# Optimization experiments

Measured on AMD Instinct MI355X. Metric: run time of the kernel, lower is better.

The kernel has to match this reference:

```python
import jax, jax.numpy as jnp
import numpy as np

EMBED = 768
FFN = 3072
HEADS = 12
HEAD_DIM = EMBED // HEADS
B, T = 4, 2048


def _layer_norm(x, g, b, eps=1e-5):
    m = jnp.mean(x, axis=-1, keepdims=True)
    v = jnp.mean((x - m) ** 2, axis=-1, keepdims=True)
    return (x - m) * jax.lax.rsqrt(v + eps) * g + b


def setup_inputs() -> dict:
    key = jax.random.key(0)
    ks = jax.random.split(key, 8)
    s_e = 1.0 / np.sqrt(EMBED)
    s_f = 1.0 / np.sqrt(FFN)
    # weights stored [in, out] (transpose of torch Linear layout)
    return {
        "x": jax.random.normal(ks[0], (B, T, EMBED), dtype=jnp.float32),
        "ln1_g": jnp.ones((EMBED,), jnp.float32),
        "ln1_b": jnp.zeros((EMBED,), jnp.float32),
        "wq": jax.random.uniform(ks[1], (EMBED, EMBED), jnp.float32, -s_e, s_e),
        "bq": jnp.zeros((EMBED,), jnp.float32),
        "wk": jax.random.uniform(ks[2], (EMBED, EMBED), jnp.float32, -s_e, s_e),
        "bk": jnp.zeros((EMBED,), jnp.float32),
        "wv": jax.random.uniform(ks[3], (EMBED, EMBED), jnp.float32, -s_e, s_e),
        "bv": jnp.zeros((EMBED,), jnp.float32),
        "wo": jax.random.uniform(ks[4], (EMBED, EMBED), jnp.float32, -s_e, s_e),
        "bo": jnp.zeros((EMBED,), jnp.float32),
        "ln2_g": jnp.ones((EMBED,), jnp.float32),
        "ln2_b": jnp.zeros((EMBED,), jnp.float32),
        "w1": jax.random.uniform(ks[5], (EMBED, FFN), jnp.float32, -s_e, s_e),
        "b1": jnp.zeros((FFN,), jnp.float32),
        "w2": jax.random.uniform(ks[6], (FFN, EMBED), jnp.float32, -s_f, s_f),
        "b2": jnp.zeros((EMBED,), jnp.float32),
    }


def reference(x, ln1_g, ln1_b, wq, bq, wk, bk, wv, bv, wo, bo,
              ln2_g, ln2_b, w1, b1, w2, b2):
    Bx, Tx, C = x.shape
    # --- self-attention block (pre-norm) ---
    residual = x
    h = _layer_norm(x, ln1_g, ln1_b)
    q = (h @ wq + bq).reshape(Bx, Tx, HEADS, HEAD_DIM)
    k = (h @ wk + bk).reshape(Bx, Tx, HEADS, HEAD_DIM)
    v = (h @ wv + bv).reshape(Bx, Tx, HEADS, HEAD_DIM)
    scale = 1.0 / np.sqrt(HEAD_DIM)
    attn = jnp.einsum('bqhd,bkhd->bhqk', q, k) * scale  # [B,H,T,T]
    attn = jax.nn.softmax(attn, axis=-1)
    o = jnp.einsum('bhqk,bkhd->bqhd', attn, v).reshape(Bx, Tx, C)
    x = residual + (o @ wo + bo)
    # --- FFN block (pre-norm) ---
    residual = x
    h = _layer_norm(x, ln2_g, ln2_b)
    h = jax.nn.gelu(h @ w1 + b1, approximate=False)
    x = residual + (h @ w2 + b2)
    return x
```

## Files before the change

kernel.cpp:

```cpp
#include <hip/hip_runtime.h>
#include <hip/hip_bf16.h>

#define EMBED 768
#define FFNDIM 3072
#define HEADS 12
#define HDIM  64
#define BB    4
#define TT    2048
#define MTOK  (BB*TT)

typedef __hip_bfloat16 bf16;
typedef __attribute__((ext_vector_type(8))) short short8;
typedef __attribute__((ext_vector_type(4))) float f32x4;
typedef __attribute__((ext_vector_type(16))) float f32x16;
typedef __attribute__((ext_vector_type(4))) unsigned short ushort4v;

__device__ __forceinline__ f32x4 mfma16(short8 a, short8 b, f32x4 c) {
  return __builtin_amdgcn_mfma_f32_16x16x32_bf16(a, b, c, 0, 0, 0);
}
__device__ __forceinline__ f32x16 mfma32(short8 a, short8 b, f32x16 c) {
  return __builtin_amdgcn_mfma_f32_32x32x16_bf16(a, b, c, 0, 0, 0);
}

__device__ __forceinline__ unsigned short f2bf(float f) {
  union { float f; unsigned int u; } v; v.f = f;
  unsigned int u = v.u;
  return (unsigned short)((u + 0x7fffu + ((u >> 16) & 1u)) >> 16);
}

__device__ __forceinline__ float fexp2(float x) {
#if __has_builtin(__builtin_amdgcn_exp2f)
  return __builtin_amdgcn_exp2f(x);
#else
  return exp2f(x);
#endif
}

__device__ __forceinline__ float gelu_f(float v) {
  const float ax = fabsf(v) * 0.70710678118f;
  const float t = __builtin_amdgcn_rcpf(1.f + 0.3275911f * ax);
  float p = 1.061405429f;
  p = p * t - 1.453152027f;
  p = p * t + 1.421413741f;
  p = p * t - 0.284496736f;
  p = p * t + 0.254829592f;
  p = p * t;
  const float e = fexp2(-ax * ax * 1.4426950408889634f);
  float er = 1.f - p * e;
  er = (v < 0.f) ? -er : er;
  return 0.5f * v * (1.f + er);
}

__device__ __forceinline__ unsigned cvtpk(float lo, float hi) {
  unsigned r;
  asm("v_cvt_pk_bf16_f32 %0, %1, %2" : "=v"(r) : "v"(lo), "v"(hi));
  return r;
}
__device__ __forceinline__ void pl32swap(unsigned& vdst, unsigned& vsrc) {
  asm("v_permlane32_swap_b32 %0, %1" : "+v"(vdst), "+v"(vsrc));
}

__device__ __forceinline__ void gl_lds16(const void* g, void* l) {
  __builtin_amdgcn_global_load_lds((const __attribute__((address_space(1))) void*)g,
                                   (__attribute__((address_space(3))) void*)l, 16, 0, 0);
}

template <int N>
__device__ __forceinline__ void wait_vm() {
  asm volatile("s_waitcnt vmcnt(%0)" :: "i"(N) : "memory");
  __builtin_amdgcn_sched_barrier(0);
}
__device__ __forceinline__ void block_barrier() {
  __builtin_amdgcn_sched_barrier(0);
  __builtin_amdgcn_s_barrier();
  __builtin_amdgcn_sched_barrier(0);
}

#define QSCALE 0.18033688011112042f
#define DEFER_THR 11.54f

struct TArgs {
  const float* src[6];
  bf16* dst[6];
  int K[6];
  int N[6];
};

__global__ __launch_bounds__(256) void transpose_k(TArgs ta) {
  const int mi = blockIdx.z;
  const int K = ta.K[mi], N = ta.N[mi];
  const int nt = N / 32;
  const int bx = blockIdx.x % nt, by = blockIdx.x / nt;
  const int n0 = bx * 32, k0 = by * 32;
  if (k0 >= K) return;
  __shared__ float t[32][33];
  const float* __restrict__ W = ta.src[mi];
  bf16* __restrict__ Wt = ta.dst[mi];
  const int tx = threadIdx.x & 31, ty = threadIdx.x >> 5;
#pragma unroll
  for (int i = 0; i < 4; ++i) {
    int kk = ty + i * 8;
    t[tx][kk] = W[(size_t)(k0 + kk) * N + n0 + tx];
  }
  __syncthreads();
#pragma unroll
  for (int i = 0; i < 4; ++i) {
    int nn = ty + i * 8;
    Wt[(size_t)(n0 + nn) * K + k0 + tx] = __float2bfloat16(t[nn][tx]);
  }
}

__global__ __launch_bounds__(256) void ln_k(const float* __restrict__ x,
                                            const float* __restrict__ g,
                                            const float* __restrict__ b,
                                            bf16* __restrict__ out) {
  const int row = blockIdx.x * 4 + (threadIdx.x >> 6);
  const int lane = threadIdx.x & 63;
  const float* xr = x + (size_t)row * EMBED;
  float4 v[3];
  float s = 0.f;
#pragma unroll
  for (int i = 0; i < 3; ++i) {
    v[i] = *(const float4*)&xr[i * 256 + lane * 4];
    s += v[i].x + v[i].y + v[i].z + v[i].w;
  }
#pragma unroll
  for (int m = 1; m < 64; m <<= 1) s += __shfl_xor(s, m);
  const float mean = s * (1.f / 768.f);
  float ss = 0.f;
#pragma unroll
  for (int i = 0; i < 3; ++i) {
    float dx = v[i].x - mean, dy = v[i].y - mean, dz = v[i].z - mean, dw = v[i].w - mean;
    ss += dx * dx + dy * dy + dz * dz + dw * dw;
  }
#pragma unroll
  for (int m = 1; m < 64; m <<= 1) ss += __shfl_xor(ss, m);
  const float rstd = rsqrtf(ss * (1.f / 768.f) + 1e-5f);
#pragma unroll
  for (int i = 0; i < 3; ++i) {
    float4 g4 = *(const float4*)&g[i * 256 + lane * 4];
    float4 b4 = *(const float4*)&b[i * 256 + lane * 4];
    ushort4v o4;
    o4[0] = f2bf((v[i].x - mean) * rstd * g4.x + b4.x);
    o4[1] = f2bf((v[i].y - mean) * rstd * g4.y + b4.y);
    o4[2] = f2bf((v[i].z - mean) * rstd * g4.z + b4.z);
    o4[3] = f2bf((v[i].w - mean) * rstd * g4.w + b4.w);
    *(ushort4v*)&out[(size_t)row * EMBED + i * 256 + lane * 4] = o4;
  }
}

template <int EPI, int TN>
__global__ __launch_bounds__(256) void gemm_bt_k(
    const bf16* __restrict__ A, const bf16* __restrict__ Bt,
    const float* __restrict__ bias, const float* __restrict__ bias2,
    const float* __restrict__ bias3, const float* __restrict__ resid,
    float* __restrict__ outf, bf16* __restrict__ outb,
    bf16* __restrict__ outk, bf16* __restrict__ outvt,
    int N, int K) {
  constexpr int MI = (TN == 128) ? 4 : 2;
  constexpr int SN = (TN == 128) ? 4 : 3;
  constexpr int ABUF = 128 * 32;
  constexpr int BBUF = TN * 32;
  __shared__ __align__(16) bf16 smem[3 * ABUF + 3 * BBUF];
  bf16* Al = smem;
  bf16* Bl = smem + 3 * ABUF;

  const int tid = threadIdx.x;
  const int lane = tid & 63;
  const int w = tid >> 6;
  const int l16 = lane & 15, g = lane >> 4;
  const int wrbase = (TN == 128) ? (w >> 1) * 64 : w * 32;
  const int wcbase = (TN == 128) ? (w & 1) * 64 : 0;

  const int nbx = N / TN;
  const int logical = ((int)blockIdx.x & 7) * ((int)gridDim.x >> 3) + ((int)blockIdx.x >> 3);
  const int m0 = (logical / nbx) * 128, n0 = (logical % nbx) * TN;

  f32x4 acc[MI][4];
#pragma unroll
  for (int i = 0; i < MI; ++i)
#pragma unroll
    for (int j = 0; j < 4; ++j) acc[i][j] = {0.f, 0.f, 0.f, 0.f};

  const int st_r = lane >> 2;
  const int st_c = ((lane & 3) ^ ((lane >> 3) & 3)) * 8;
  const size_t a_base = (size_t)(m0 + w * 32) * K;
  const size_t b_base = (TN == 128) ? (size_t)(n0 + w * 32) * K
                                    : (size_t)(n0 + w * 16) * K;

  auto stage = [&](int bufi, int kt) {
#pragma unroll
    for (int p = 0; p < 2; ++p)
      gl_lds16(A + a_base + (size_t)(p * 16 + st_r) * K + kt + st_c,
               &Al[bufi * ABUF + (w * 32 + p * 16) * 32]);
    if constexpr (TN == 128) {
#pragma unroll
      for (int p = 0; p < 2; ++p)
        gl_lds16(Bt + b_base + (size_t)(p * 16 + st_r) * K + kt + st_c,
                 &Bl[bufi * BBUF + (w * 32 + p * 16) * 32]);
    } else {
      gl_lds16(Bt + b_base + (size_t)st_r * K + kt + st_c, &Bl[bufi * BBUF + (w * 16) * 32]);
    }
  };

  const int nt = K >> 5;
  stage(0, 0);
  stage(1, 32);
  const int sw = (l16 >> 1) & 3;
  int buf = 0;
  for (int t = 0; t < nt; ++t) {
    if (t < nt - 1) wait_vm<SN>(); else wait_vm<0>();
    block_barrier();
    if (t + 2 < nt) {
      int nb = buf + 2; if (nb >= 3) nb -= 3;
      stage(nb, (t + 2) * 32);
    }
    short8 af[MI], bfr[4];
#pragma unroll
    for (int i = 0; i < MI; ++i)
      af[i] = *(const short8*)&Al[buf * ABUF + (wrbase + i * 16 + l16) * 32 + (g ^ sw) * 8];
#pragma unroll
    for (int j = 0; j < 4; ++j)
      bfr[j] = *(const short8*)&Bl[buf * BBUF + (wcbase + j * 16 + l16) * 32 + (g ^ sw) * 8];
#pragma unroll
    for (int i = 0; i < MI; ++i)
#pragma unroll
      for (int j = 0; j < 4; ++j) acc[i][j] = mfma16(af[i], bfr[j], acc[i][j]);
    buf = (buf == 2) ? 0 : buf + 1;
  }

  const int crow = m0 + wrbase + g * 4;
  const int ccol = n0 + wcbase + l16;

  if constexpr (EPI == 0) {
    const int region = n0 / EMBED;
    const float* bp = (region == 0) ? bias : (region == 1) ? bias2 : bias3;
    if (region < 2) {
      const float sc = (region == 0) ? QSCALE : 1.0f;
      bf16* __restrict__ dstb = (region == 0) ? outb : outk;
      __syncthreads();
      bf16* S = smem;
#pragma unroll
      for (int j = 0; j < 4; ++j) {
        const int cn = ccol - region * EMBED + j * 16;
        const float bvv = bp[cn];
        const int nl = wcbase + j * 16 + l16;
#pragma unroll
        for (int i = 0; i < MI; ++i)
#pragma unroll
          for (int rr = 0; rr < 4; ++rr) {
            const int mlcl = wrbase + i * 16 + g * 4 + rr;
            S[mlcl * 128 + (nl ^ ((mlcl & 15) << 3))] =
                __float2bfloat16((acc[i][j][rr] + bvv) * sc);
          }
      }
      __syncthreads();
      const int colbase = n0 - region * EMBED;
#pragma unroll
      for (int pp = 0; pp < 8; ++pp) {
        const int m_l = pp * 16 + (tid >> 4);
        const int c = tid & 15;
        short8 vv = *(const short8*)&S[m_l * 128 + ((c ^ (m_l & 15)) << 3)];
        *(short8*)&dstb[(size_t)(m0 + m_l) * EMBED + colbase + c * 8] = vv;
      }
    } else {
      __syncthreads();
      constexpr int SP = 136;
      bf16* S = smem;
#pragma unroll
      for (int j = 0; j < 4; ++j) {
        const int cn = ccol - 2 * EMBED + j * 16;
        const float bvv = bp[cn];
        const int nl = wcbase + j * 16 + l16;
#pragma unroll
        for (int i = 0; i < MI; ++i) {
          ushort4v pk;
#pragma unroll
          for (int rr = 0; rr < 4; ++rr) pk[rr] = f2bf(acc[i][j][rr] + bvv);
          *(ushort4v*)&S[nl * SP + wrbase + i * 16 + g * 4] = pk;
        }
      }
      __syncthreads();
      const int row = tid >> 1;
      const int hm = tid & 1;
      const int cn2 = n0 - 2 * EMBED + row;
      const int hh = cn2 >> 6, dd = cn2 & 63;
      const int bb2 = m0 >> 11;
      const int t0 = (m0 & 2047) + hm * 64;
      bf16* __restrict__ dst = &outvt[((size_t)((bb2 * HEADS + hh) * HDIM + dd)) * TT + t0];
      const bf16* src = &S[row * SP + hm * 64];
#pragma unroll
      for (int kk = 0; kk < 8; ++kk)
        *(short8*)&dst[kk * 8] = *(const short8*)&src[kk * 8];
    }
  } else if constexpr (EPI == 1) {
    constexpr int SW = TN + 4;
    float* S32 = (float*)smem;
    const int mychunk = w >> 1;
#pragma unroll
    for (int c = 0; c < 2; ++c) {
      __syncthreads();
      if (mychunk == c) {
        const int rbase = wrbase - c * 64;
#pragma unroll
        for (int j = 0; j < 4; ++j) {
          const int nl = wcbase + j * 16 + l16;
          const float bvv = bias[n0 + nl];
#pragma unroll
          for (int i = 0; i < MI; ++i)
#pragma unroll
            for (int rr = 0; rr < 4; ++rr)
              S32[(rbase + i * 16 + g * 4 + rr) * SW + nl] = acc[i][j][rr] + bvv;
        }
      }
      __syncthreads();
      if constexpr (TN == 128) {
#pragma unroll
        for (int p = 0; p < 8; ++p) {
          const int rowc = p * 8 + (tid >> 5);
          const int c4 = (tid & 31) * 4;
          const int m = m0 + c * 64 + rowc;
          float4 rv = *(const float4*)&resid[(size_t)m * N + n0 + c4];
          const float* sp = &S32[rowc * SW + c4];
          float4 ov;
          ov.x = rv.x + sp[0]; ov.y = rv.y + sp[1];
          ov.z = rv.z + sp[2]; ov.w = rv.w + sp[3];
          *(float4*)&outf[(size_t)m * N + n0 + c4] = ov;
        }
      } else {
#pragma unroll
        for (int p = 0; p < 4; ++p) {
          const int rowc = p * 16 + (tid >> 4);
          const int c4 = (tid & 15) * 4;
          const int m = m0 + c * 64 + rowc;
          float4 rv = *(const float4*)&resid[(size_t)m * N + n0 + c4];
          const float* sp = &S32[rowc * SW + c4];
          float4 ov;
          ov.x = rv.x + sp[0]; ov.y = rv.y + sp[1];
          ov.z = rv.z + sp[2]; ov.w = rv.w + sp[3];
          *(float4*)&outf[(size_t)m * N + n0 + c4] = ov;
        }
      }
    }
  } else {
    __syncthreads();
    bf16* S = smem;
#pragma unroll
    for (int j = 0; j < 4; ++j) {
      const int cn = ccol + j * 16;
      const float bvv = bias[cn];
      const int nl = wcbase + j * 16 + l16;
#pragma unroll
      for (int i = 0; i < MI; ++i)
#pragma unroll
        for (int rr = 0; rr < 4; ++rr) {
          const int mlcl = wrbase + i * 16 + g * 4 + rr;
          S[mlcl * 128 + (nl ^ ((mlcl & 15) << 3))] =
              __float2bfloat16(gelu_f(acc[i][j][rr] + bvv));
        }
    }
    __syncthreads();
#pragma unroll
    for (int pp = 0; pp < 8; ++pp) {
      const int m_l = pp * 16 + (tid >> 4);
      const int c = tid & 15;
      short8 vv = *(const short8*)&S[m_l * 128 + ((c ^ (m_l & 15)) << 3)];
      *(short8*)&outb[(size_t)(m0 + m_l) * N + n0 + c * 8] = vv;
    }
  }
}

__global__ __launch_bounds__(256, 4) void flash9_k(const bf16* __restrict__ q,
                                                   const bf16* __restrict__ k,
                                                   const bf16* __restrict__ vt,
                                                   bf16* __restrict__ po,
                                                   float2* __restrict__ ml) {
  const int tid = threadIdx.x, lane = tid & 63;
  const int l32 = lane & 31, hl = lane >> 5;
  const int w = tid >> 6;
  const int logical = ((int)blockIdx.x & 7) * 192 + ((int)blockIdx.x >> 3);
  const int qt = logical & 15;
  const int rest = logical >> 4;
  const int half = rest & 1;
  const int hb = rest >> 1;
  const int h = hb % HEADS, b = hb / HEADS;
  const int q0 = (qt * 4 + w) * 32;
  const int kv0 = half * (TT / 2);

  __shared__ bf16 Kl[2][64 * 64];
  __shared__ bf16 Vl[2][64 * 64];

  short8 qf[4];
  {
    const bf16* qp = q + (size_t)(b * TT + q0 + l32) * EMBED + h * HDIM + hl * 8;
#pragma unroll
    for (int c = 0; c < 4; ++c) qf[c] = *(const short8*)&qp[c * 16];
  }

  const bf16* __restrict__ kgs = k + (size_t)(b * TT) * EMBED + h * HDIM;
  const bf16* __restrict__ vgs = vt + ((size_t)((b * HEADS + h) * HDIM)) * TT;

  f32x16 oacc0, oacc1;
#pragma unroll
  for (int i = 0; i < 16; ++i) { oacc0[i] = 0.f; oacc1[i] = 0.f; }
  float mrun = -1.0e30f, lrun = 0.f;

  const int st_rw = w * 8 + (lane >> 3);
  const int st_cs0 = lane & 7;
  auto stage = [&](int buf, int kv) {
#pragma unroll
    for (int p = 0; p < 2; ++p) {
      const int r = p * 32 + st_rw;
      const int cs = st_cs0 ^ (r & 7);
      char* kdst = (char*)&Kl[buf][0] + p * 4096 + w * 1024;
      char* vdst = (char*)&Vl[buf][0] + p * 4096 + w * 1024;
      gl_lds16(kgs + (size_t)(kv + r) * EMBED + cs * 8, kdst);
      gl_lds16(vgs + (size_t)r * TT + kv + cs * 8, vdst);
    }
  };

  auto subtile = [&](int buf, int s2) {
    const int krow = s2 * 32 + l32;
    const char* Kb = (const char*)&Kl[buf][0];
    const char* Vb = (const char*)&Vl[buf][0];
    short8 kf[4];
#pragma unroll
    for (int c = 0; c < 4; ++c)
      kf[c] = *(const short8*)(Kb + krow * 128 + (((2 * c + hl) ^ (krow & 7)) * 16));

    f32x16 s;
#pragma unroll
    for (int i = 0; i < 16; ++i) s[i] = 0.f;
    __builtin_amdgcn_s_setprio(1);
#pragma unroll
    for (int c = 0; c < 4; ++c) s = mfma32(kf[c], qf[c], s);
    __builtin_amdgcn_s_setprio(0);

    float m0 = fmaxf(fmaxf(s[0], s[1]), s[2]);
    float m1 = fmaxf(fmaxf(s[3], s[4]), s[5]);
    float m2 = fmaxf(fmaxf(s[6], s[7]), s[8]);
    float m3 = fmaxf(fmaxf(s[9], s[10]), s[11]);
    float m4 = fmaxf(fmaxf(s[12], s[13]), s[14]);
    float mx = fmaxf(fmaxf(fmaxf(m0, m1), fmaxf(m2, m3)), fmaxf(m4, s[15]));
    mx = fmaxf(mx, __shfl_xor(mx, 32));

    if (!__all(mx <= mrun + DEFER_THR)) {
      const float mn = fmaxf(mrun, mx);
      const float al = fexp2(mrun - mn);
      lrun *= al;
#pragma unroll
      for (int i = 0; i < 16; ++i) { oacc0[i] *= al; oacc1[i] *= al; }
      mrun = mn;
    }

#pragma unroll
    for (int i = 0; i < 16; ++i) s[i] = fexp2(s[i] - mrun);
    float a8[8];
#pragma unroll
    for (int i = 0; i < 8; ++i) a8[i] = s[2 * i] + s[2 * i + 1];
    float ps = ((a8[0] + a8[1]) + (a8[2] + a8[3])) + ((a8[4] + a8[5]) + (a8[6] + a8[7]));
    ps += __shfl_xor(ps, 32);
    lrun += ps;

    union { unsigned u[4]; short8 s8; } pa0, pa1;
    {
      unsigned U = cvtpk(s[0], s[1]), V = cvtpk(s[4], s[5]);
      pl32swap(V, U); pa0.u[0] = U; pa0.u[2] = V;
      unsigned U1 = cvtpk(s[2], s[3]), V1 = cvtpk(s[6], s[7]);
      pl32swap(V1, U1); pa0.u[1] = U1; pa0.u[3] = V1;
    }
    {
      unsigned U = cvtpk(s[8], s[9]), V = cvtpk(s[12], s[13]);
      pl32swap(V, U); pa1.u[0] = U; pa1.u[2] = V;
      unsigned U1 = cvtpk(s[10], s[11]), V1 = cvtpk(s[14], s[15]);
      pl32swap(V1, U1); pa1.u[1] = U1; pa1.u[3] = V1;
    }

    short8 vf[4];
#pragma unroll
    for (int ks = 0; ks < 2; ++ks)
#pragma unroll
      for (int dc = 0; dc < 2; ++dc) {
        const int vrow = dc * 32 + l32;
        vf[ks * 2 + dc] = *(const short8*)(
            Vb + vrow * 128 + (((s2 * 4 + ks * 2 + hl) ^ (vrow & 7)) * 16));
      }

    __builtin_amdgcn_s_setprio(1);
    oacc0 = mfma32(vf[0], pa0.s8, oacc0);
    oacc0 = mfma32(vf[2], pa1.s8, oacc0);
    oacc1 = mfma32(vf[1], pa0.s8, oacc1);
    oacc1 = mfma32(vf[3], pa1.s8, oacc1);
    __builtin_amdgcn_s_setprio(0);
  };

  const int NT = (TT / 2) / 64;
  stage(0, kv0);
  __syncthreads();
  int buf = 0;
  for (int t = 0; t < NT; ++t) {
    if (t + 1 < NT) stage(buf ^ 1, kv0 + (t + 1) * 64);
    subtile(buf, 0);
    subtile(buf, 1);
    __syncthreads();
    buf ^= 1;
  }

  bf16* pp = po + ((size_t)((half * BB + b) * HEADS + h) * TT + q0 + l32) * 64;
#pragma unroll
  for (int a = 0; a < 4; ++a) {
    ushort4v pk4;
#pragma unroll
    for (int bb = 0; bb < 4; ++bb) pk4[bb] = f2bf(oacc0[a * 4 + bb]);
    *(ushort4v*)&pp[a * 8 + hl * 4] = pk4;
#pragma unroll
    for (int bb = 0; bb < 4; ++bb) pk4[bb] = f2bf(oacc1[a * 4 + bb]);
    *(ushort4v*)&pp[32 + a * 8 + hl * 4] = pk4;
  }
  if (hl == 0) {
    float2 v2; v2.x = mrun; v2.y = lrun;
    ml[(size_t)((half * BB + b) * HEADS + h) * TT + q0 + l32] = v2;
  }
}

__global__ __launch_bounds__(256) void combine_k(const bf16* __restrict__ po,
                                                 const float2* __restrict__ ml,
                                                 bf16* __restrict__ o) {
  const int row = blockIdx.x * 4 + (threadIdx.x >> 6);
  const int lane = threadIdx.x & 63;
  const size_t NR = (size_t)BB * HEADS * TT;
  const float2 a = ml[row];
  const float2 c = ml[NR + row];
  const float M = fmaxf(a.x, c.x);
  const float w0 = fexp2(a.x - M), w1 = fexp2(c.x - M);
  const float inv = 1.f / (w0 * a.y + w1 * c.y);
  const float o0 = __bfloat162float(po[(size_t)row * 64 + lane]);
  const float o1 = __bfloat162float(po[NR * 64 + (size_t)row * 64 + lane]);
  const float val = (w0 * o0 + w1 * o1) * inv;
  const int b = row / (HEADS * TT);
  const int rem = row % (HEADS * TT);
  const int h = rem / TT, t = rem % TT;
  o[((size_t)(b * TT + t)) * EMBED + h * HDIM + lane] = __float2bfloat16(val);
}

extern "C" void kernel_launch(void* const* d_in, const int* in_sizes, int n_in,
                              void* d_out, int out_size, void* d_ws,
                              size_t ws_size, hipStream_t stream) {
  const float* x = (const float*)d_in[0];
  const float* ln1g = (const float*)d_in[1];
  const float* ln1b = (const float*)d_in[2];
  const float* wq = (const float*)d_in[3];
  const float* bq = (const float*)d_in[4];
  const float* wk = (const float*)d_in[5];
  const float* bk = (const float*)d_in[6];
  const float* wv = (const float*)d_in[7];
  const float* bv = (const float*)d_in[8];
  const float* wo = (const float*)d_in[9];
  const float* bo = (const float*)d_in[10];
  const float* ln2g = (const float*)d_in[11];
  const float* ln2b = (const float*)d_in[12];
  const float* w1 = (const float*)d_in[13];
  const float* b1 = (const float*)d_in[14];
  const float* w2 = (const float*)d_in[15];
  const float* b2 = (const float*)d_in[16];
  float* out = (float*)d_out;

  char* ws = (char*)d_ws;
  size_t off = 0;
  auto alloc = [&](size_t bytes) {
    char* p = ws + off;
    off += (bytes + 255) & ~(size_t)255;
    return p;
  };
  bf16* wqkv_t = (bf16*)alloc((size_t)2304 * 768 * 2);
  bf16* wo_t = (bf16*)alloc((size_t)768 * 768 * 2);
  bf16* w1_t = (bf16*)alloc((size_t)3072 * 768 * 2);
  bf16* w2_t = (bf16*)alloc((size_t)768 * 3072 * 2);
  bf16* h = (bf16*)alloc((size_t)MTOK * EMBED * 2);
  char* qkvo = alloc((size_t)MTOK * EMBED * 2 * 4);
  bf16* qb = (bf16*)qkvo;
  bf16* kb = qb + (size_t)MTOK * EMBED;
  bf16* vtb = kb + (size_t)MTOK * EMBED;
  bf16* ob = vtb + (size_t)MTOK * EMBED;
  bf16* h1 = (bf16*)qkvo;
  float* x1 = (float*)alloc((size_t)MTOK * EMBED * 4);
  (void)ws_size;
  bf16* po = (bf16*)x1;
  float2* mlb = (float2*)h;

  TArgs ta;
  ta.src[0] = wq; ta.dst[0] = wqkv_t;                  ta.K[0] = 768;  ta.N[0] = 768;
  ta.src[1] = wk; ta.dst[1] = wqkv_t + 768 * 768;      ta.K[1] = 768;  ta.N[1] = 768;
  ta.src[2] = wv; ta.dst[2] = wqkv_t + 2 * 768 * 768;  ta.K[2] = 768;  ta.N[2] = 768;
  ta.src[3] = wo; ta.dst[3] = wo_t;                    ta.K[3] = 768;  ta.N[3] = 768;
  ta.src[4] = w1; ta.dst[4] = w1_t;                    ta.K[4] = 768;  ta.N[4] = 3072;
  ta.src[5] = w2; ta.dst[5] = w2_t;                    ta.K[5] = 3072; ta.N[5] = 768;

  transpose_k<<<dim3(2304, 1, 6), dim3(256), 0, stream>>>(ta);
  ln_k<<<dim3(MTOK / 4), dim3(256), 0, stream>>>(x, ln1g, ln1b, h);
  gemm_bt_k<0, 128><<<dim3((2304 / 128) * (MTOK / 128)), dim3(256), 0, stream>>>(
      h, wqkv_t, bq, bk, bv, nullptr, nullptr, qb, kb, vtb, 2304, 768);
  flash9_k<<<dim3(16 * HEADS * BB * 2), dim3(256), 0, stream>>>(qb, kb, vtb, po, mlb);
  combine_k<<<dim3(BB * HEADS * TT / 4), dim3(256), 0, stream>>>(po, mlb, ob);
  gemm_bt_k<1, 64><<<dim3((768 / 64) * (MTOK / 128)), dim3(256), 0, stream>>>(
      ob, wo_t, bo, nullptr, nullptr, x, x1, nullptr, nullptr, nullptr, 768, 768);
  ln_k<<<dim3(MTOK / 4), dim3(256), 0, stream>>>(x1, ln2g, ln2b, h);
  gemm_bt_k<2, 128><<<dim3((3072 / 128) * (MTOK / 128)), dim3(256), 0, stream>>>(
      h, w1_t, b1, nullptr, nullptr, nullptr, nullptr, h1, nullptr, nullptr, 3072, 768);
  gemm_bt_k<1, 128><<<dim3((768 / 128) * (MTOK / 128)), dim3(256), 0, stream>>>(
      h1, w2_t, b2, nullptr, nullptr, x1, out, nullptr, nullptr, nullptr, 768, 3072);
}
```

Baseline: 292.1 us.

## Write Q/K/V in MFMA fragment order and load flash operands directly from global

The QKV GEMM epilogue now scatters Q, K and V into a fragment-ordered layout that matches the per-lane MFMA operand pattern. The attention kernel then reads K and V fragments straight from global memory with contiguous 16-byte loads per lane. This removes LDS staging, double buffering and block barriers from the attention loop. The cost is that each wave fetches K/V independently, raising L2 traffic, and there is no explicit prefetch left to hide global load latency.

New measurement: 289.5 us. About the same (-0.9%).

```diff
diff --git a/kernel.cpp b/kernel.cpp
--- a/kernel.cpp
+++ b/kernel.cpp
@@ -78,6 +78,7 @@
 
 #define QSCALE 0.18033688011112042f
 #define DEFER_THR 11.54f
+
 
 struct TArgs {
   const float* src[6];
@@ -235,9 +236,11 @@
   if constexpr (EPI == 0) {
     const int region = n0 / EMBED;
     const float* bp = (region == 0) ? bias : (region == 1) ? bias2 : bias3;
+    const int bb2 = m0 >> 11;
+    const int kb0 = (m0 & 2047) >> 5;
     if (region < 2) {
       const float sc = (region == 0) ? QSCALE : 1.0f;
-      bf16* __restrict__ dstb = (region == 0) ? outb : outk;
+      bf16* __restrict__ fb = (region == 0) ? outb : outk;
       __syncthreads();
       bf16* S = smem;
 #pragma unroll
@@ -255,13 +258,23 @@
           }
       }
       __syncthreads();
-      const int colbase = n0 - region * EMBED;
-#pragma unroll
-      for (int pp = 0; pp < 8; ++pp) {
-        const int m_l = pp * 16 + (tid >> 4);
-        const int c = tid & 15;
-        short8 vv = *(const short8*)&S[m_l * 128 + ((c ^ (m_l & 15)) << 3)];
-        *(short8*)&dstb[(size_t)(m0 + m_l) * EMBED + colbase + c * 8] = vv;
+      const int hbase = (n0 - region * EMBED) >> 6;
+#pragma unroll
+      for (int gg = 0; gg < 8; ++gg) {
+        const int rid = gg * 256 + tid;
+        const int hp = rid >> 10;
+        const int rest2 = rid & 1023;
+        const int kbc = rest2 >> 6;
+        const int kbl = kbc >> 2, c = kbc & 3;
+        const int lid = rest2 & 63;
+        const int hl = lid >> 5, l32r = lid & 31;
+        const int m_l = kbl * 32 + l32r;
+        const int nl = hp * 64 + c * 16 + hl * 8;
+        short8 vv = *(const short8*)&S[m_l * 128 + (nl ^ ((m_l & 15) << 3))];
+        const size_t fidx =
+            ((((size_t)(bb2 * HEADS + hbase + hp) * 64 + kb0 + kbl) * 4 + c) * 64 +
+             lid) * 8;
+        *(short8*)&fb[fidx] = vv;
       }
     } else {
       __syncthreads();
@@ -281,17 +294,25 @@
         }
       }
       __syncthreads();
-      const int row = tid >> 1;
-      const int hm = tid & 1;
-      const int cn2 = n0 - 2 * EMBED + row;
-      const int hh = cn2 >> 6, dd = cn2 & 63;
-      const int bb2 = m0 >> 11;
-      const int t0 = (m0 & 2047) + hm * 64;
-      bf16* __restrict__ dst = &outvt[((size_t)((bb2 * HEADS + hh) * HDIM + dd)) * TT + t0];
-      const bf16* src = &S[row * SP + hm * 64];
-#pragma unroll
-      for (int kk = 0; kk < 8; ++kk)
-        *(short8*)&dst[kk * 8] = *(const short8*)&src[kk * 8];
+      const int hbase = (n0 - 2 * EMBED) >> 6;
+#pragma unroll
+      for (int gg = 0; gg < 8; ++gg) {
+        const int rid = gg * 256 + tid;
+        const int hp = rid >> 10;
+        const int rest2 = rid & 1023;
+        const int kbl = rest2 >> 8;
+        const int ks = (rest2 >> 7) & 1;
+        const int dc = (rest2 >> 6) & 1;
+        const int hl = (rest2 >> 5) & 1;
+        const int l32r = rest2 & 31;
+        const int nl = hp * 64 + dc * 32 + l32r;
+        const int m_l = kbl * 32 + ks * 16 + hl * 8;
+        short8 vv = *(const short8*)&S[nl * SP + m_l];
+        const size_t fidx =
+            ((((size_t)(bb2 * HEADS + hbase + hp) * 64 + kb0 + kbl) * 8 + ks * 4 +
+              dc * 2 + hl) * 32 + l32r) * 8;
+        *(short8*)&outvt[fidx] = vv;
+      }
     }
   } else if constexpr (EPI == 1) {
     constexpr int SW = TN + 4;
@@ -370,11 +391,11 @@
   }
 }
 
-__global__ __launch_bounds__(256, 4) void flash9_k(const bf16* __restrict__ q,
-                                                   const bf16* __restrict__ k,
-                                                   const bf16* __restrict__ vt,
-                                                   bf16* __restrict__ po,
-                                                   float2* __restrict__ ml) {
+__global__ __launch_bounds__(256, 4) void flash11_k(const bf16* __restrict__ qfb,
+                                                    const bf16* __restrict__ kfb,
+                                                    const bf16* __restrict__ vfb,
+                                                    bf16* __restrict__ po,
+                                                    float2* __restrict__ ml) {
   const int tid = threadIdx.x, lane = tid & 63;
   const int l32 = lane & 31, hl = lane >> 5;
   const int w = tid >> 6;
@@ -384,49 +405,30 @@
   const int half = rest & 1;
   const int hb = rest >> 1;
   const int h = hb % HEADS, b = hb / HEADS;
-  const int q0 = (qt * 4 + w) * 32;
+  const int qbi = qt * 4 + w;
   const int kv0 = half * (TT / 2);
-
-  __shared__ bf16 Kl[2][64 * 64];
-  __shared__ bf16 Vl[2][64 * 64];
+  const size_t bh = (size_t)(b * HEADS + h);
 
   short8 qf[4];
   {
-    const bf16* qp = q + (size_t)(b * TT + q0 + l32) * EMBED + h * HDIM + hl * 8;
-#pragma unroll
-    for (int c = 0; c < 4; ++c) qf[c] = *(const short8*)&qp[c * 16];
-  }
-
-  const bf16* __restrict__ kgs = k + (size_t)(b * TT) * EMBED + h * HDIM;
-  const bf16* __restrict__ vgs = vt + ((size_t)((b * HEADS + h) * HDIM)) * TT;
+    const bf16* qp = qfb + ((bh * 64 + qbi) * 4) * 512 + lane * 8;
+#pragma unroll
+    for (int c = 0; c < 4; ++c) qf[c] = *(const short8*)&qp[c * 512];
+  }
+  const bf16* __restrict__ kbb = kfb + bh * 64 * 2048;
+  const bf16* __restrict__ vbb = vfb + bh * 64 * 2048;
 
   f32x16 oacc0, oacc1;
 #pragma unroll
   for (int i = 0; i < 16; ++i) { oacc0[i] = 0.f; oacc1[i] = 0.f; }
   float mrun = -1.0e30f, lrun = 0.f;
 
-  const int st_rw = w * 8 + (lane >> 3);
-  const int st_cs0 = lane & 7;
-  auto stage = [&](int buf, int kv) {
-#pragma unroll
-    for (int p = 0; p < 2; ++p) {
-      const int r = p * 32 + st_rw;
-      const int cs = st_cs0 ^ (r & 7);
-      char* kdst = (char*)&Kl[buf][0] + p * 4096 + w * 1024;
-      char* vdst = (char*)&Vl[buf][0] + p * 4096 + w * 1024;
-      gl_lds16(kgs + (size_t)(kv + r) * EMBED + cs * 8, kdst);
-      gl_lds16(vgs + (size_t)r * TT + kv + cs * 8, vdst);
-    }
-  };
-
-  auto subtile = [&](int buf, int s2) {
-    const int krow = s2 * 32 + l32;
-    const char* Kb = (const char*)&Kl[buf][0];
-    const char* Vb = (const char*)&Vl[buf][0];
+  auto subtile = [&](int kvabs) {
+    const int kb = kvabs >> 5;
+    const bf16* kp = kbb + (size_t)kb * 2048 + lane * 8;
     short8 kf[4];
 #pragma unroll
-    for (int c = 0; c < 4; ++c)
-      kf[c] = *(const short8*)(Kb + krow * 128 + (((2 * c + hl) ^ (krow & 7)) * 16));
+    for (int c = 0; c < 4; ++c) kf[c] = *(const short8*)&kp[c * 512];
 
     f32x16 s;
 #pragma unroll
@@ -476,15 +478,13 @@
       pl32swap(V1, U1); pa1.u[1] = U1; pa1.u[3] = V1;
     }
 
+    const bf16* vp = vbb + (size_t)kb * 2048 + lane * 8;
     short8 vf[4];
 #pragma unroll
     for (int ks = 0; ks < 2; ++ks)
 #pragma unroll
-      for (int dc = 0; dc < 2; ++dc) {
-        const int vrow = dc * 32 + l32;
-        vf[ks * 2 + dc] = *(const short8*)(
-            Vb + vrow * 128 + (((s2 * 4 + ks * 2 + hl) ^ (vrow & 7)) * 16));
-      }
+      for (int dc = 0; dc < 2; ++dc)
+        vf[ks * 2 + dc] = *(const short8*)&vp[(ks * 4 + dc * 2) * 256];
 
     __builtin_amdgcn_s_setprio(1);
     oacc0 = mfma32(vf[0], pa0.s8, oacc0);
@@ -495,17 +495,13 @@
   };
 
   const int NT = (TT / 2) / 64;
-  stage(0, kv0);
-  __syncthreads();
-  int buf = 0;
   for (int t = 0; t < NT; ++t) {
-    if (t + 1 < NT) stage(buf ^ 1, kv0 + (t + 1) * 64);
-    subtile(buf, 0);
-    subtile(buf, 1);
-    __syncthreads();
-    buf ^= 1;
-  }
-
+    const int base = kv0 + t * 64;
+    subtile(base);
+    subtile(base + 32);
+  }
+
+  const int q0 = qbi * 32;
   bf16* pp = po + ((size_t)((half * BB + b) * HEADS + h) * TT + q0 + l32) * 64;
 #pragma unroll
   for (int a = 0; a < 4; ++a) {
@@ -600,7 +596,7 @@
   ln_k<<<dim3(MTOK / 4), dim3(256), 0, stream>>>(x, ln1g, ln1b, h);
   gemm_bt_k<0, 128><<<dim3((2304 / 128) * (MTOK / 128)), dim3(256), 0, stream>>>(
       h, wqkv_t, bq, bk, bv, nullptr, nullptr, qb, kb, vtb, 2304, 768);
-  flash9_k<<<dim3(16 * HEADS * BB * 2), dim3(256), 0, stream>>>(qb, kb, vtb, po, mlb);
+  flash11_k<<<dim3(16 * HEADS * BB * 2), dim3(256), 0, stream>>>(qb, kb, vtb, po, mlb);
   combine_k<<<dim3(BB * HEADS * TT / 4), dim3(256), 0, stream>>>(po, mlb, ob);
   gemm_bt_k<1, 64><<<dim3((768 / 64) * (MTOK / 128)), dim3(256), 0, stream>>>(
       ob, wo_t, bo, nullptr, nullptr, x, x1, nullptr, nullptr, nullptr, 768, 768);
```
